# Performance work log

Measured on AMD Instinct MI355X. Metric: run time of the kernel, lower is better.

The kernel has to match this reference:

```python
import jax, jax.numpy as jnp
import numpy as np

SIGMA = 1.0

def setup_inputs() -> dict:
    key = jax.random.key(0)
    k1, k2 = jax.random.split(key)
    N, IN, OUT = 524288, 64, 128
    x = jax.random.normal(k1, (N, IN), dtype=jnp.float32)
    bin_centers = jax.random.normal(k2, (OUT, IN), dtype=jnp.float32)
    return {"x": x, "bin_centers": bin_centers}

def reference(x, bin_centers):
    # distances[n,o] = sum_i (x[n,i] - c[o,i])^2 = ||x_n||^2 - 2 x_n.c_o + ||c_o||^2
    x2 = jnp.sum(x * x, axis=1)[:, None]                # [N,1]
    c2 = jnp.sum(bin_centers * bin_centers, axis=1)[None, :]  # [1,O]
    xc = jnp.einsum('ni,oi->no', x, bin_centers)        # [N,O] GEMM
    distances = x2 - 2.0 * xc + c2                      # [N,O]
    rbf = jnp.exp(-distances / (2.0 * SIGMA ** 2))      # [N,O]
    # histogram[o,i] = sum_n rbf[n,o] * x[n,i]  ->  rbf^T @ x
    histogram = jnp.einsum('no,ni->oi', rbf, x)         # [O,I] GEMM
    return histogram
```

## Files before the change

kernel.cpp:

```cpp
#include <hip/hip_runtime.h>
#include <stdint.h>


typedef _Float16 half8v __attribute__((ext_vector_type(8)));
typedef _Float16 half4v __attribute__((ext_vector_type(4)));
typedef __fp16  fp16x2 __attribute__((ext_vector_type(2)));
typedef float floatx4 __attribute__((ext_vector_type(4)));

#define GRIDN 512
#define NITER 32
#define LOG2E 1.4426950408889634f
#define PBIAS 38.0f
#define PUNSCALE 3.637978807091713e-12f

#if __has_builtin(__builtin_amdgcn_exp2f)
#define EXP2F(x) __builtin_amdgcn_exp2f(x)
#else
#define EXP2F(x) exp2f(x)
#endif

static __device__ __forceinline__ unsigned int pk16z(float a, float b) {
  fp16x2 h = __builtin_amdgcn_cvt_pkrtz(a, b);
  return __builtin_bit_cast(unsigned int, h);
}
static __device__ __forceinline__ unsigned int pk16(float a, float b) {
  unsigned short ha = __builtin_bit_cast(unsigned short, (_Float16)a);
  unsigned short hb = __builtin_bit_cast(unsigned short, (_Float16)b);
  return (unsigned int)ha | ((unsigned int)hb << 16);
}
static __device__ __forceinline__ half4v mkh4(unsigned int lo, unsigned int hi) {
  uint2 u{lo, hi};
  return __builtin_bit_cast(half4v, u);
}
static __device__ __forceinline__ half8v mkh8(unsigned int a, unsigned int b,
                                              unsigned int c, unsigned int d) {
  uint4 u{a, b, c, d};
  return __builtin_bit_cast(half8v, u);
}

static __device__ __forceinline__ floatx4 mfma32(half8v a, half8v b, floatx4 c) {
  return __builtin_amdgcn_mfma_f32_16x16x32_f16(a, b, c, 0, 0, 0);
}
static __device__ __forceinline__ floatx4 mfma16(half4v a, half4v b, floatx4 c) {
  return __builtin_amdgcn_mfma_f32_16x16x16f16(a, b, c, 0, 0, 0);
}

#define LSTR 72

__global__ __launch_bounds__(256, 4) void rbf_hist_kernel(
    const float* __restrict__ x, const float* __restrict__ c,
    float* __restrict__ out) {
  __shared__ unsigned short sXh[32][LSTR];
  __shared__ float          sX2[32];

  const int t    = threadIdx.x;
  const int lane = t & 63;
  const int w    = t >> 6;
  const int l15  = lane & 15;
  const int quad = lane >> 4;

  half8v chi[2][2];
  float m2c[2];
#pragma unroll
  for (int oo = 0; oo < 2; ++oo) {
    const int ot = 2 * w + oo;
    float sq = 0.f;
#pragma unroll
    for (int s = 0; s < 2; ++s) {
      const float* p = c + (ot * 16 + l15) * 64 + s * 32 + quad * 8;
      float4 va = *(const float4*)(p);
      float4 vb = *(const float4*)(p + 4);
      float f[8] = {va.x, va.y, va.z, va.w, vb.x, vb.y, vb.z, vb.w};
      unsigned int h[4];
#pragma unroll
      for (int jp = 0; jp < 4; ++jp) {
        float a = f[2 * jp], b = f[2 * jp + 1];
        sq = fmaf(a, a, sq);
        sq = fmaf(b, b, sq);
        h[jp] = pk16(a * LOG2E, b * LOG2E);
      }
      chi[oo][s] = mkh8(h[0], h[1], h[2], h[3]);
    }
    sq += __shfl_xor(sq, 16);
    sq += __shfl_xor(sq, 32);
    m2c[oo] = fmaf(-0.5f * LOG2E, sq, PBIAS);
  }

  half4v iden;
  {
    float e0 = (quad * 4 + 0 == l15) ? 1.f : 0.f;
    float e1 = (quad * 4 + 1 == l15) ? 1.f : 0.f;
    float e2 = (quad * 4 + 2 == l15) ? 1.f : 0.f;
    float e3 = (quad * 4 + 3 == l15) ? 1.f : 0.f;
    iden = mkh4(pk16z(e0, e1), pk16z(e2, e3));
  }

  floatx4 hacc[2][4];
#pragma unroll
  for (int a = 0; a < 2; ++a)
#pragma unroll
    for (int b = 0; b < 4; ++b) {
      floatx4 z = {0.f, 0.f, 0.f, 0.f};
      hacc[a][b] = z;
    }

  const int r = t >> 3, q = t & 7;

  float4 vA[2], vB[2];
  {
    const float* pA = x + ((size_t)blockIdx.x * 32 + r) * 64 + q * 8;
    vA[0] = *(const float4*)(pA);
    vA[1] = *(const float4*)(pA + 4);
    const float* pB =
        x + ((size_t)(blockIdx.x + GRIDN) * 32 + r) * 64 + q * 8;
    vB[0] = *(const float4*)(pB);
    vB[1] = *(const float4*)(pB + 4);
  }

#pragma unroll 1
  for (int it = 0; it < NITER; it += 2) {
#pragma unroll
    for (int par = 0; par < 2; ++par) {
      float4* v = (par == 0) ? vA : vB;

      __syncthreads();

      {
        float f0 = v[0].x, f1 = v[0].y, f2 = v[0].z, f3 = v[0].w;
        float f4 = v[1].x, f5 = v[1].y, f6 = v[1].z, f7 = v[1].w;
        float sq = 0.f;
        sq = fmaf(f0, f0, sq); sq = fmaf(f1, f1, sq);
        sq = fmaf(f2, f2, sq); sq = fmaf(f3, f3, sq);
        sq = fmaf(f4, f4, sq); sq = fmaf(f5, f5, sq);
        sq = fmaf(f6, f6, sq); sq = fmaf(f7, f7, sq);
        *(uint4*)&sXh[r][q * 8] =
            uint4{pk16(f0, f1), pk16(f2, f3), pk16(f4, f5), pk16(f6, f7)};
        sq += __shfl_xor(sq, 1);
        sq += __shfl_xor(sq, 2);
        sq += __shfl_xor(sq, 4);
        if (q == 0) sX2[r] = -0.5f * LOG2E * sq;
      }
      __syncthreads();

      if (it + par + 2 < NITER) {
        const float* p = x +
            ((size_t)(blockIdx.x + (it + par + 2) * GRIDN) * 32 + r) * 64 +
            q * 8;
        v[0] = *(const float4*)(p);
        v[1] = *(const float4*)(p + 4);
      }

#pragma unroll
      for (int t2 = 0; t2 < 2; ++t2) {
        half8v xh0 = *(const half8v*)&sXh[t2 * 16 + l15][quad * 8];
        half8v xh1 = *(const half8v*)&sXh[t2 * 16 + l15][32 + quad * 8];
        float4 m2x = *(const float4*)&sX2[t2 * 16 + quad * 4];

        half4v P[2];
#pragma unroll
        for (int oo = 0; oo < 2; ++oo) {
          floatx4 acc = {m2x.x + m2c[oo], m2x.y + m2c[oo],
                         m2x.z + m2c[oo], m2x.w + m2c[oo]};
          acc = mfma32(xh0, chi[oo][0], acc);
          acc = mfma32(xh1, chi[oo][1], acc);
          P[oo] = mkh4(pk16z(EXP2F(acc[0]), EXP2F(acc[1])),
                       pk16z(EXP2F(acc[2]), EXP2F(acc[3])));
        }

        half4v XT[4];
#pragma unroll
        for (int itl = 0; itl < 4; ++itl) {
          half4v ax = *(const half4v*)&sXh[t2 * 16 + l15][itl * 16 + quad * 4];
          floatx4 z = {0.f, 0.f, 0.f, 0.f};
          floatx4 d = mfma16(ax, iden, z);
          XT[itl] = mkh4(pk16z(d[0], d[1]), pk16z(d[2], d[3]));
        }

#pragma unroll
        for (int oo = 0; oo < 2; ++oo)
#pragma unroll
          for (int itl = 0; itl < 4; ++itl)
            hacc[oo][itl] = mfma16(P[oo], XT[itl], hacc[oo][itl]);
      }
    }
  }

#pragma unroll
  for (int oo = 0; oo < 2; ++oo)
#pragma unroll
    for (int itl = 0; itl < 4; ++itl)
#pragma unroll
      for (int e = 0; e < 4; ++e) {
        int o = (2 * w + oo) * 16 + quad * 4 + e;
        int i = itl * 16 + l15;
        atomicAdd(out + o * 64 + i, hacc[oo][itl][e] * PUNSCALE);
      }
}

__global__ void zero_out_kernel(float* out, int n) {
  int i = blockIdx.x * 256 + threadIdx.x;
  if (i < n) out[i] = 0.f;
}

extern "C" void kernel_launch(void* const* d_in, const int* in_sizes, int n_in,
                              void* d_out, int out_size, void* d_ws, size_t ws_size,
                              hipStream_t stream) {
  (void)in_sizes; (void)n_in; (void)d_ws; (void)ws_size;
  const float* x = (const float*)d_in[0];
  const float* c = (const float*)d_in[1];
  float* out = (float*)d_out;

  zero_out_kernel<<<(out_size + 255) / 256, 256, 0, stream>>>(out, out_size);
  rbf_hist_kernel<<<GRIDN, 256, 0, stream>>>(x, c, out);
}
```

Baseline: 198.1 us.

## Double-buffer staged x tile in LDS to halve barriers per tile

```diff
diff --git a/kernel.cpp b/kernel.cpp
--- a/kernel.cpp
+++ b/kernel.cpp
@@ -50,8 +50,8 @@
 __global__ __launch_bounds__(256, 4) void rbf_hist_kernel(
     const float* __restrict__ x, const float* __restrict__ c,
     float* __restrict__ out) {
-  __shared__ unsigned short sXh[32][LSTR];
-  __shared__ float          sX2[32];
+  __shared__ unsigned short sXh[2][32][LSTR];
+  __shared__ float          sX2[2][32];
 
   const int t    = threadIdx.x;
   const int lane = t & 63;
@@ -106,82 +106,102 @@
 
   const int r = t >> 3, q = t & 7;
 
-  float4 vA[2], vB[2];
+  auto stage = [&](int B, float4 v0, float4 v1) {
+    float f0 = v0.x, f1 = v0.y, f2 = v0.z, f3 = v0.w;
+    float f4 = v1.x, f5 = v1.y, f6 = v1.z, f7 = v1.w;
+    float sq = 0.f;
+    sq = fmaf(f0, f0, sq); sq = fmaf(f1, f1, sq);
+    sq = fmaf(f2, f2, sq); sq = fmaf(f3, f3, sq);
+    sq = fmaf(f4, f4, sq); sq = fmaf(f5, f5, sq);
+    sq = fmaf(f6, f6, sq); sq = fmaf(f7, f7, sq);
+    *(uint4*)&sXh[B][r][q * 8] =
+        uint4{pk16(f0, f1), pk16(f2, f3), pk16(f4, f5), pk16(f6, f7)};
+    sq += __shfl_xor(sq, 1);
+    sq += __shfl_xor(sq, 2);
+    sq += __shfl_xor(sq, 4);
+    if (q == 0) sX2[B][r] = -0.5f * LOG2E * sq;
+  };
+
+  auto compute = [&](int B) {
+#pragma unroll
+    for (int t2 = 0; t2 < 2; ++t2) {
+      half8v xh0 = *(const half8v*)&sXh[B][t2 * 16 + l15][quad * 8];
+      half8v xh1 = *(const half8v*)&sXh[B][t2 * 16 + l15][32 + quad * 8];
+      float4 m2x = *(const float4*)&sX2[B][t2 * 16 + quad * 4];
+
+      half4v P[2];
+#pragma unroll
+      for (int oo = 0; oo < 2; ++oo) {
+        floatx4 acc = {m2x.x + m2c[oo], m2x.y + m2c[oo],
+                       m2x.z + m2c[oo], m2x.w + m2c[oo]};
+        acc = mfma32(xh0, chi[oo][0], acc);
+        acc = mfma32(xh1, chi[oo][1], acc);
+        P[oo] = mkh4(pk16z(EXP2F(acc[0]), EXP2F(acc[1])),
+                     pk16z(EXP2F(acc[2]), EXP2F(acc[3])));
+      }
+
+      half4v XT[4];
+#pragma unroll
+      for (int itl = 0; itl < 4; ++itl) {
+        half4v ax = *(const half4v*)&sXh[B][t2 * 16 + l15][itl * 16 + quad * 4];
+        floatx4 z = {0.f, 0.f, 0.f, 0.f};
+        floatx4 d = mfma16(ax, iden, z);
+        XT[itl] = mkh4(pk16z(d[0], d[1]), pk16z(d[2], d[3]));
+      }
+
+#pragma unroll
+      for (int oo = 0; oo < 2; ++oo)
+#pragma unroll
+        for (int itl = 0; itl < 4; ++itl)
+          hacc[oo][itl] = mfma16(P[oo], XT[itl], hacc[oo][itl]);
+    }
+  };
+
   {
-    const float* pA = x + ((size_t)blockIdx.x * 32 + r) * 64 + q * 8;
-    vA[0] = *(const float4*)(pA);
-    vA[1] = *(const float4*)(pA + 4);
+    const float* p0 = x + ((size_t)blockIdx.x * 32 + r) * 64 + q * 8;
+    float4 a0 = *(const float4*)(p0);
+    float4 a1 = *(const float4*)(p0 + 4);
+    const float* p1 =
+        x + ((size_t)(blockIdx.x + GRIDN) * 32 + r) * 64 + q * 8;
+    float4 b0 = *(const float4*)(p1);
+    float4 b1 = *(const float4*)(p1 + 4);
+    stage(0, a0, a1);
+    stage(1, b0, b1);
+  }
+  float4 rA[2], rB[2];
+  {
+    const float* pA =
+        x + ((size_t)(blockIdx.x + 2 * GRIDN) * 32 + r) * 64 + q * 8;
+    rA[0] = *(const float4*)(pA);
+    rA[1] = *(const float4*)(pA + 4);
     const float* pB =
-        x + ((size_t)(blockIdx.x + GRIDN) * 32 + r) * 64 + q * 8;
-    vB[0] = *(const float4*)(pB);
-    vB[1] = *(const float4*)(pB + 4);
-  }
+        x + ((size_t)(blockIdx.x + 3 * GRIDN) * 32 + r) * 64 + q * 8;
+    rB[0] = *(const float4*)(pB);
+    rB[1] = *(const float4*)(pB + 4);
+  }
+  __syncthreads();
 
 #pragma unroll 1
   for (int it = 0; it < NITER; it += 2) {
-#pragma unroll
-    for (int par = 0; par < 2; ++par) {
-      float4* v = (par == 0) ? vA : vB;
-
-      __syncthreads();
-
-      {
-        float f0 = v[0].x, f1 = v[0].y, f2 = v[0].z, f3 = v[0].w;
-        float f4 = v[1].x, f5 = v[1].y, f6 = v[1].z, f7 = v[1].w;
-        float sq = 0.f;
-        sq = fmaf(f0, f0, sq); sq = fmaf(f1, f1, sq);
-        sq = fmaf(f2, f2, sq); sq = fmaf(f3, f3, sq);
-        sq = fmaf(f4, f4, sq); sq = fmaf(f5, f5, sq);
-        sq = fmaf(f6, f6, sq); sq = fmaf(f7, f7, sq);
-        *(uint4*)&sXh[r][q * 8] =
-            uint4{pk16(f0, f1), pk16(f2, f3), pk16(f4, f5), pk16(f6, f7)};
-        sq += __shfl_xor(sq, 1);
-        sq += __shfl_xor(sq, 2);
-        sq += __shfl_xor(sq, 4);
-        if (q == 0) sX2[r] = -0.5f * LOG2E * sq;
-      }
-      __syncthreads();
-
-      if (it + par + 2 < NITER) {
-        const float* p = x +
-            ((size_t)(blockIdx.x + (it + par + 2) * GRIDN) * 32 + r) * 64 +
-            q * 8;
-        v[0] = *(const float4*)(p);
-        v[1] = *(const float4*)(p + 4);
-      }
-
-#pragma unroll
-      for (int t2 = 0; t2 < 2; ++t2) {
-        half8v xh0 = *(const half8v*)&sXh[t2 * 16 + l15][quad * 8];
-        half8v xh1 = *(const half8v*)&sXh[t2 * 16 + l15][32 + quad * 8];
-        float4 m2x = *(const float4*)&sX2[t2 * 16 + quad * 4];
-
-        half4v P[2];
-#pragma unroll
-        for (int oo = 0; oo < 2; ++oo) {
-          floatx4 acc = {m2x.x + m2c[oo], m2x.y + m2c[oo],
-                         m2x.z + m2c[oo], m2x.w + m2c[oo]};
-          acc = mfma32(xh0, chi[oo][0], acc);
-          acc = mfma32(xh1, chi[oo][1], acc);
-          P[oo] = mkh4(pk16z(EXP2F(acc[0]), EXP2F(acc[1])),
-                       pk16z(EXP2F(acc[2]), EXP2F(acc[3])));
-        }
-
-        half4v XT[4];
-#pragma unroll
-        for (int itl = 0; itl < 4; ++itl) {
-          half4v ax = *(const half4v*)&sXh[t2 * 16 + l15][itl * 16 + quad * 4];
-          floatx4 z = {0.f, 0.f, 0.f, 0.f};
-          floatx4 d = mfma16(ax, iden, z);
-          XT[itl] = mkh4(pk16z(d[0], d[1]), pk16z(d[2], d[3]));
-        }
-
-#pragma unroll
-        for (int oo = 0; oo < 2; ++oo)
-#pragma unroll
-          for (int itl = 0; itl < 4; ++itl)
-            hacc[oo][itl] = mfma16(P[oo], XT[itl], hacc[oo][itl]);
-      }
+    compute(0);
+    __syncthreads();
+    if (it + 2 < NITER) stage(0, rA[0], rA[1]);
+    if (it + 4 < NITER) {
+      const float* p = x +
+          ((size_t)(blockIdx.x + (size_t)(it + 4) * GRIDN) * 32 + r) * 64 +
+          q * 8;
+      rA[0] = *(const float4*)(p);
+      rA[1] = *(const float4*)(p + 4);
+    }
+    compute(1);
+    __syncthreads();
+    if (it + 3 < NITER) stage(1, rB[0], rB[1]);
+    if (it + 5 < NITER) {
+      const float* p = x +
+          ((size_t)(blockIdx.x + (size_t)(it + 5) * GRIDN) * 32 + r) * 64 +
+          q * 8;
+      rB[0] = *(const float4*)(p);
+      rB[1] = *(const float4*)(p + 4);
     }
   }
 
```

Result: no change. 199.8 us (+0.9%).
